# Kernel tuning notes

Hardware: AMD Instinct MI355X
Metric: run time of the kernel (lower is better)

## Reference

```python
import jax, jax.numpy as jnp
import numpy as np

B, DIM, HEADS, AGENT = 16, 256, 8, 49
POOL = 7  # int(sqrt(agent_num))


def _pool_matrix(size, out):
    # PyTorch AdaptiveAvgPool2d bin boundaries: start=floor(i*size/out), end=ceil((i+1)*size/out)
    P = np.zeros((out, size), np.float32)
    for i in range(out):
        s = (i * size) // out
        e = -((-(i + 1) * size) // out)
        P[i, s:e] = 1.0 / (e - s)
    return jnp.asarray(P)


def _forward(x, Wq, Wkv, Wproj, bproj, Wdwc, bdwc,
             an_bias, na_bias, ah_bias, aw_bias, ha_bias, wa_bias, H, W):
    b, c, h, w = x.shape
    n = H * W
    head_dim = c // HEADS
    scale = head_dim ** -0.5
    xt = x.reshape(b, c, n).transpose(0, 2, 1)            # [b, n, c]
    q = xt @ Wq.T                                          # [b, n, c]
    kv = xt @ Wkv.T
    k, v = jnp.split(kv, 2, axis=-1)
    # agent tokens: adaptive avg pool of q over the HxW grid -> 7x7
    qimg = q.reshape(b, H, W, c)
    Ph, Pw = _pool_matrix(H, POOL), _pool_matrix(W, POOL)
    agent = jnp.einsum('ph,qw,bhwc->bpqc', Ph, Pw, qimg).reshape(b, AGENT, c)

    def to_heads(t):
        return t.reshape(b, -1, HEADS, head_dim).transpose(0, 2, 1, 3)

    qh, kh, vh, ah = to_heads(q), to_heads(k), to_heads(v), to_heads(agent)

    # stage 1: agent -> kv attention with interpolated position bias
    pb1 = jax.image.resize(an_bias, (HEADS, AGENT, H, W), method='bilinear').reshape(HEADS, AGENT, n)
    pb2 = (ah_bias + aw_bias).reshape(1, HEADS, AGENT, n)
    pos_bias = pb1[None] + pb2                             # [1/b, h, 49, n]
    agent_attn = jax.nn.softmax(jnp.einsum('bhad,bhnd->bhan', ah * scale, kh) + pos_bias, axis=-1)
    agent_v = jnp.einsum('bhan,bhnd->bhad', agent_attn, vh)  # [b, h, 49, d]

    # stage 2: query -> agent attention
    ab1 = jax.image.resize(na_bias, (HEADS, AGENT, H, W), method='bilinear').reshape(HEADS, AGENT, n).transpose(0, 2, 1)
    ab2 = (ha_bias + wa_bias).reshape(1, HEADS, n, AGENT)
    agent_bias = ab1[None] + ab2                           # [1/b, h, n, 49]
    q_attn = jax.nn.softmax(jnp.einsum('bhnd,bhad->bhna', qh * scale, ah) + agent_bias, axis=-1)
    out = jnp.einsum('bhna,bhad->bhnd', q_attn, agent_v).transpose(0, 2, 1, 3).reshape(b, n, c)

    # depthwise conv residual on v
    vimg = vh.transpose(0, 2, 1, 3).reshape(b, H, W, c).transpose(0, 3, 1, 2)  # [b, c, H, W]
    dw = jax.lax.conv_general_dilated(vimg, Wdwc, (1, 1), 'SAME',
                                      feature_group_count=c,
                                      dimension_numbers=('NCHW', 'OIHW', 'NCHW'))
    dw = dw + bdwc[None, :, None, None]
    out = out + dw.transpose(0, 2, 3, 1).reshape(b, n, c)
    out = out @ Wproj.T + bproj
    return out.transpose(0, 2, 1).reshape(b, c, h, w)


def setup_inputs() -> dict:
    key = jax.random.key(0)
    ks = jax.random.split(key, 12)
    s = 0.02
    return {
        'x': jax.random.normal(ks[0], (B, DIM, 64, 64), jnp.float32),
        'Wq': jax.random.normal(ks[1], (DIM, DIM), jnp.float32) * s,
        'Wkv': jax.random.normal(ks[2], (2 * DIM, DIM), jnp.float32) * s,
        'Wproj': jax.random.normal(ks[3], (DIM, DIM), jnp.float32) * s,
        'bproj': jnp.zeros((DIM,), jnp.float32),
        'Wdwc': jax.random.normal(ks[4], (DIM, 1, 3, 3), jnp.float32) * s,
        'bdwc': jnp.zeros((DIM,), jnp.float32),
        'an_bias': jax.random.normal(ks[5], (HEADS, AGENT, 7, 7), jnp.float32) * s,
        'na_bias': jax.random.normal(ks[6], (HEADS, AGENT, 7, 7), jnp.float32) * s,
        'ah_bias': jax.random.normal(ks[7], (1, HEADS, AGENT, 64, 1), jnp.float32) * s,
        'aw_bias': jax.random.normal(ks[8], (1, HEADS, AGENT, 1, 64), jnp.float32) * s,
        'ha_bias': jax.random.normal(ks[9], (1, HEADS, 64, 1, AGENT), jnp.float32) * s,
        'wa_bias': jax.random.normal(ks[10], (1, HEADS, 1, 64, AGENT), jnp.float32) * s,
        'H': 64,
        'W': 64,
    }


def reference(x, Wq, Wkv, Wproj, bproj, Wdwc, bdwc,
              an_bias, na_bias, ah_bias, aw_bias, ha_bias, wa_bias, H, W):
    return _forward(x, Wq, Wkv, Wproj, bproj, Wdwc, bdwc,
                    an_bias, na_bias, ah_bias, aw_bias, ha_bias, wa_bias, H, W)
```

## Files before the change

kernel.cpp:

```cpp
#include <hip/hip_runtime.h>
#include <hip/hip_bf16.h>
#include <stdint.h>

using bf16 = __hip_bfloat16;

#define SCALE 0.17677669529663687f

typedef short short8 __attribute__((ext_vector_type(8)));
typedef float f32x4 __attribute__((ext_vector_type(4)));

__device__ __forceinline__ float bf2f(bf16 v) { return __bfloat162float(v); }

__device__ __forceinline__ unsigned short f2bf(float f) {
    unsigned int u = __float_as_uint(f);
    unsigned int r = u + 0x7fffu + ((u >> 16) & 1u);
    return (unsigned short)(r >> 16);
}

__device__ __forceinline__ void load8bf(const bf16* p, float* f) {
    uint4 u = *reinterpret_cast<const uint4*>(p);
    f[0] = __uint_as_float(u.x << 16); f[1] = __uint_as_float(u.x & 0xffff0000u);
    f[2] = __uint_as_float(u.y << 16); f[3] = __uint_as_float(u.y & 0xffff0000u);
    f[4] = __uint_as_float(u.z << 16); f[5] = __uint_as_float(u.z & 0xffff0000u);
    f[6] = __uint_as_float(u.w << 16); f[7] = __uint_as_float(u.w & 0xffff0000u);
}

__device__ __forceinline__ void gload16(const void* g, void* l) {
    __builtin_amdgcn_global_load_lds(
        (const __attribute__((address_space(1))) void*)g,
        (__attribute__((address_space(3))) void*)l, 16, 0, 0);
}

__global__ __launch_bounds__(256) void convert_w(
    const float* __restrict__ Wq, const float* __restrict__ Wkv,
    const float* __restrict__ Wp,
    bf16* __restrict__ Wqkv_bf, bf16* __restrict__ Wp_bf)
{
    int row = blockIdx.x, tid = threadIdx.x;
    const float* src; bf16* dst;
    if (row < 768) {
        src = (row < 256) ? Wq + (size_t)row * 256 : Wkv + (size_t)(row - 256) * 256;
        dst = Wqkv_bf + (size_t)row * 256;
    } else {
        src = Wp + (size_t)(row - 768) * 256;
        dst = Wp_bf + (size_t)(row - 768) * 256;
    }
    *reinterpret_cast<unsigned short*>(dst + tid) = f2bf(src[tid]);
}

__global__ __launch_bounds__(256) void x_to_bf16T(
    const float* __restrict__ x, bf16* __restrict__ xT)
{
    __shared__ float t[64][65];
    const int b = blockIdx.z, pos0 = blockIdx.x * 64, c0 = blockIdx.y * 64;
    const int tid = threadIdx.x;
    const int cc = tid >> 6, p = tid & 63;
    #pragma unroll
    for (int i = 0; i < 16; ++i)
        t[cc + 4 * i][p] = x[((size_t)(b * 256 + c0 + cc + 4 * i)) * 4096 + pos0 + p];
    __syncthreads();
    const int pl = tid >> 2, qd = tid & 3;
    unsigned short tmp[16];
    #pragma unroll
    for (int j = 0; j < 16; ++j) tmp[j] = f2bf(t[qd * 16 + j][pl]);
    uint4* dst = reinterpret_cast<uint4*>(xT + ((size_t)(b * 4096 + pos0 + pl)) * 256 + c0 + qd * 16);
    dst[0] = reinterpret_cast<const uint4*>(tmp)[0];
    dst[1] = reinterpret_cast<const uint4*>(tmp)[1];
}

__global__ __launch_bounds__(256) void qkv_mfma(
    const bf16* __restrict__ xT, const bf16* __restrict__ Wqkv,
    bf16* __restrict__ q, bf16* __restrict__ k, bf16* __restrict__ v)
{
    __shared__ __align__(16) short As[128 * 32];
    __shared__ __align__(16) short Bs[128 * 32];
    const int b = blockIdx.x >> 5;
    const int m0 = (blockIdx.x & 31) * 128;
    const int j0 = blockIdx.y * 128;
    const int tid = threadIdx.x;
    const int w = tid >> 6, lane = tid & 63;
    const int wm = w & 1, wn = w >> 1;
    const int quad = lane >> 4, ln = lane & 15;

    const short* Ag = (const short*)xT + ((size_t)(b * 4096 + m0)) * 256;
    const short* Bg = (const short*)Wqkv + (size_t)j0 * 256;
    const int ldrow = lane >> 2;
    const int ldcol = (lane & 3) * 8;

    f32x4 acc[4][4] = {};

    for (int k0 = 0; k0 < 256; k0 += 32) {
        __syncthreads();
        #pragma unroll
        for (int p = 0; p < 2; ++p) {
            int row = w * 32 + p * 16;
            gload16(Ag + (size_t)(row + ldrow) * 256 + k0 + ldcol, As + row * 32);
            gload16(Bg + (size_t)(row + ldrow) * 256 + k0 + ldcol, Bs + row * 32);
        }
        __syncthreads();
        short8 af[4], bfr[4];
        #pragma unroll
        for (int mi = 0; mi < 4; ++mi)
            af[mi] = *reinterpret_cast<const short8*>(&As[(wm * 64 + mi * 16 + ln) * 32 + quad * 8]);
        #pragma unroll
        for (int ni = 0; ni < 4; ++ni)
            bfr[ni] = *reinterpret_cast<const short8*>(&Bs[(wn * 64 + ni * 16 + ln) * 32 + quad * 8]);
        #pragma unroll
        for (int mi = 0; mi < 4; ++mi)
            #pragma unroll
            for (int ni = 0; ni < 4; ++ni)
                acc[mi][ni] = __builtin_amdgcn_mfma_f32_16x16x32_bf16(
                    af[mi], bfr[ni], acc[mi][ni], 0, 0, 0);
    }

    bf16* dst; int cb;
    if (j0 < 256)      { dst = q; cb = j0; }
    else if (j0 < 512) { dst = k; cb = j0 - 256; }
    else               { dst = v; cb = j0 - 512; }
    #pragma unroll
    for (int mi = 0; mi < 4; ++mi)
        #pragma unroll
        for (int r = 0; r < 4; ++r) {
            int pos = m0 + wm * 64 + mi * 16 + quad * 4 + r;
            unsigned short* o = reinterpret_cast<unsigned short*>(
                dst + ((size_t)(b * 4096 + pos)) * 256 + cb + wn * 64 + ln);
            #pragma unroll
            for (int ni = 0; ni < 4; ++ni)
                o[ni * 16] = f2bf(acc[mi][ni][r]);
        }
}

__global__ __launch_bounds__(256) void pool_agent(
    const bf16* __restrict__ q, float* __restrict__ agent)
{
    int bid = blockIdx.x;
    int b = bid / 49, a = bid % 49;
    int py = a / 7, px = a % 7;
    int ys = (py * 64) / 7, ye = ((py + 1) * 64 + 6) / 7;
    int xs = (px * 64) / 7, xe = ((px + 1) * 64 + 6) / 7;
    int ch = threadIdx.x;
    float s = 0.f;
    for (int y = ys; y < ye; ++y)
        for (int x = xs; x < xe; ++x)
            s += bf2f(q[((size_t)(b * 4096) + y * 64 + x) * 256 + ch]);
    agent[((size_t)(b * 49) + a) * 256 + ch] = s / (float)((ye - ys) * (xe - xs));
}

__global__ __launch_bounds__(256) void make_pbias(
    const float* __restrict__ an, const float* __restrict__ ahb,
    const float* __restrict__ awb, float* __restrict__ pbias)
{
    int bid = blockIdx.x;
    __shared__ float bb[49], ay[64], ax[64];
    int tid = threadIdx.x;
    if (tid < 49) bb[tid] = an[(size_t)bid * 49 + tid];
    if (tid < 64) {
        ay[tid] = ahb[(size_t)bid * 64 + tid];
        ax[tid] = awb[(size_t)bid * 64 + tid];
    }
    __syncthreads();
    for (int it = 0; it < 16; ++it) {
        int pos = it * 256 + tid;
        int y = pos >> 6, x = pos & 63;
        float fy = (y + 0.5f) * (7.f / 64.f) - 0.5f; fy = fminf(fmaxf(fy, 0.f), 6.f);
        float fx = (x + 0.5f) * (7.f / 64.f) - 0.5f; fx = fminf(fmaxf(fx, 0.f), 6.f);
        int y0 = (int)fy, x0 = (int)fx;
        int y1 = min(y0 + 1, 6), x1 = min(x0 + 1, 6);
        float wy = fy - y0, wx = fx - x0;
        float val = (1.f - wy) * ((1.f - wx) * bb[y0 * 7 + x0] + wx * bb[y0 * 7 + x1])
                  + wy * ((1.f - wx) * bb[y1 * 7 + x0] + wx * bb[y1 * 7 + x1]);
        pbias[(size_t)bid * 4096 + pos] = val + ay[y] + ax[x];
    }
}

__global__ __launch_bounds__(256) void make_abias2(
    const float* __restrict__ na, const float* __restrict__ hab,
    const float* __restrict__ wab, bf16* __restrict__ ab2)
{
    const int h = blockIdx.x, p0 = blockIdx.y * 256;
    const int tid = threadIdx.x;
    __shared__ float bb[49 * 49];
    __shared__ float hy[64 * 49];
    __shared__ float wxs[64 * 49];
    for (int i = tid; i < 49 * 49; i += 256) bb[i] = na[(size_t)h * 2401 + i];
    for (int i = tid; i < 64 * 49; i += 256) {
        hy[i]  = hab[(size_t)h * 3136 + i];
        wxs[i] = wab[(size_t)h * 3136 + i];
    }
    __syncthreads();
    const int pos = p0 + tid;
    const int y = pos >> 6, x = pos & 63;
    float fy = (y + 0.5f) * (7.f / 64.f) - 0.5f; fy = fminf(fmaxf(fy, 0.f), 6.f);
    float fx = (x + 0.5f) * (7.f / 64.f) - 0.5f; fx = fminf(fmaxf(fx, 0.f), 6.f);
    int y0 = (int)fy, x0 = (int)fx;
    int y1 = min(y0 + 1, 6), x1 = min(x0 + 1, 6);
    float wy = fy - y0, wxv = fx - x0;
    float w00 = (1.f - wy) * (1.f - wxv), w01 = (1.f - wy) * wxv;
    float w10 = wy * (1.f - wxv),        w11 = wy * wxv;
    int g00 = y0 * 7 + x0, g01 = y0 * 7 + x1, g10 = y1 * 7 + x0, g11 = y1 * 7 + x1;
    unsigned short outv[64];
    #pragma unroll
    for (int a = 0; a < 49; ++a) {
        float val = w00 * bb[a * 49 + g00] + w01 * bb[a * 49 + g01]
                  + w10 * bb[a * 49 + g10] + w11 * bb[a * 49 + g11]
                  + hy[y * 49 + a] + wxs[x * 49 + a];
        outv[a] = f2bf(val);
    }
    #pragma unroll
    for (int a = 49; a < 64; ++a) outv[a] = 0;
    uint4* dst = reinterpret_cast<uint4*>(
        reinterpret_cast<unsigned short*>(ab2) + ((size_t)(h * 4096) + pos) * 64);
    #pragma unroll
    for (int j = 0; j < 8; ++j) dst[j] = reinterpret_cast<const uint4*>(outv)[j];
}

__global__ __launch_bounds__(256) void stage1(
    const float* __restrict__ agent, const bf16* __restrict__ k,
    const bf16* __restrict__ v, const float* __restrict__ pbias,
    float* __restrict__ part_O, float* __restrict__ part_sum)
{
    const int bid = blockIdx.x;
    const int split = bid & 7, h = (bid >> 3) & 7, b = bid >> 6;
    const int tid = threadIdx.x;
    const int w = tid >> 6, lane = tid & 63;
    const int ln = lane & 15, quad = lane >> 4;

    __shared__ __align__(16) short agLds[64 * 32];
    __shared__ __align__(16) short pLds[64 * 140];
    __shared__ __align__(16) short vtLds[32 * 140];

    for (int i = tid; i < 64 * 32; i += 256) {
        int a = i >> 5, d = i & 31;
        float val = (a < 49) ? agent[((size_t)(b * 49) + a) * 256 + h * 32 + d] : 0.f;
        agLds[i] = (short)f2bf(val);
    }
    __syncthreads();

    const short8 agFrag = *reinterpret_cast<const short8*>(&agLds[(w * 16 + ln) * 32 + quad * 8]);
    const int a_row = w * 16 + quad * 4;

    f32x4 oAcc[2] = {};
    float sacc[4] = {0.f, 0.f, 0.f, 0.f};
    const f32x4 zero4 = {0.f, 0.f, 0.f, 0.f};

    for (int sub = 0; sub < 4; ++sub) {
        const int nbase = split * 512 + sub * 128;
        __syncthreads();
        {
            const int n_loc = tid & 127, dh = (tid >> 7) * 16;
            const short* vr = (const short*)v + ((size_t)(b * 4096) + nbase + n_loc) * 256 + h * 32 + dh;
            uint4 u0 = *reinterpret_cast<const uint4*>(vr);
            uint4 u1 = *reinterpret_cast<const uint4*>(vr + 8);
            unsigned int uu[8] = {u0.x, u0.y, u0.z, u0.w, u1.x, u1.y, u1.z, u1.w};
            #pragma unroll
            for (int j = 0; j < 8; ++j) {
                vtLds[(dh + 2 * j) * 140 + n_loc]     = (short)(uu[j] & 0xffffu);
                vtLds[(dh + 2 * j + 1) * 140 + n_loc] = (short)(uu[j] >> 16);
            }
        }
        short8 kf[8];
        #pragma unroll
        for (int t = 0; t < 8; ++t) {
            int n = nbase + t * 16 + ln;
            kf[t] = *reinterpret_cast<const short8*>(
                (const short*)k + ((size_t)(b * 4096) + n) * 256 + h * 32 + quad * 8);
        }
        #pragma unroll
        for (int t = 0; t < 8; ++t) {
            f32x4 s = __builtin_amdgcn_mfma_f32_16x16x32_bf16(agFrag, kf[t], zero4, 0, 0, 0);
            int n = nbase + t * 16 + ln;
            #pragma unroll
            for (int r = 0; r < 4; ++r) {
                int a = a_row + r;
                float e = 0.f;
                if (a < 49) {
                    float sv = s[r] * SCALE + pbias[((size_t)(h * 49) + a) * 4096 + n];
                    e = __expf(sv);
                }
                sacc[r] += e;
                pLds[(a_row + r) * 140 + t * 16 + ln] = (short)f2bf(e);
            }
        }
        __syncthreads();
        #pragma unroll
        for (int ks = 0; ks < 4; ++ks) {
            short8 pf = *reinterpret_cast<const short8*>(&pLds[(w * 16 + ln) * 140 + ks * 32 + quad * 8]);
            #pragma unroll
            for (int dt = 0; dt < 2; ++dt) {
                short8 vf = *reinterpret_cast<const short8*>(&vtLds[(dt * 16 + ln) * 140 + ks * 32 + quad * 8]);
                oAcc[dt] = __builtin_amdgcn_mfma_f32_16x16x32_bf16(pf, vf, oAcc[dt], 0, 0, 0);
            }
        }
    }

    const size_t obase = ((size_t)((b * 8 + h) * 8 + split)) * 1568;
    #pragma unroll
    for (int dt = 0; dt < 2; ++dt)
        #pragma unroll
        for (int r = 0; r < 4; ++r) {
            int a = a_row + r;
            if (a < 49)
                part_O[obase + a * 32 + dt * 16 + ln] = oAcc[dt][r];
        }
    #pragma unroll
    for (int r = 0; r < 4; ++r) {
        float sv = sacc[r];
        #pragma unroll
        for (int m = 1; m < 16; m <<= 1) sv += __shfl_xor(sv, m, 64);
        if (ln == 0) {
            int a = a_row + r;
            if (a < 49)
                part_sum[((b * 8 + h) * 8 + split) * 49 + a] = sv;
        }
    }
}

__global__ __launch_bounds__(256) void stage1_fin(
    const float* __restrict__ part_O, const float* __restrict__ part_sum,
    bf16* __restrict__ avT)
{
    int bh = blockIdx.x;
    __shared__ float inv[49];
    int tid = threadIdx.x;
    if (tid < 49) {
        float s = 0.f;
        #pragma unroll
        for (int sp = 0; sp < 8; ++sp) s += part_sum[(bh * 8 + sp) * 49 + tid];
        inv[tid] = 1.f / s;
    }
    __syncthreads();
    unsigned short* dst = reinterpret_cast<unsigned short*>(avT) + (size_t)bh * 2048;
    for (int i = tid; i < 2048; i += 256) {
        int d = i >> 6, a = i & 63;
        float val = 0.f;
        if (a < 49) {
            float o = 0.f;
            #pragma unroll
            for (int sp = 0; sp < 8; ++sp)
                o += part_O[((size_t)(bh * 8) + sp) * 1568 + a * 32 + d];
            val = o * inv[a];
        }
        dst[i] = f2bf(val);
    }
}

__global__ __launch_bounds__(256) void stage2_mfma(
    const bf16* __restrict__ q, const bf16* __restrict__ v,
    const float* __restrict__ agent, const bf16* __restrict__ avT,
    const bf16* __restrict__ ab2, const float* __restrict__ wdwc,
    const float* __restrict__ bdwc, bf16* __restrict__ mid)
{
    const int bh = blockIdx.x;
    const int b = bh >> 3, h = bh & 7;
    const int base = blockIdx.y * 256;
    const int tid = threadIdx.x;
    const int w = tid >> 6, lane = tid & 63;
    const int quad = lane >> 4, ln = lane & 15;

    __shared__ __align__(16) short agLds[64 * 32];
    __shared__ __align__(16) short pLds[4][16 * 72];
    __shared__ __align__(16) float oLds[64 * 36];
    __shared__ float wdLds[32 * 9];
    __shared__ float bdLds[32];

    for (int i = tid; i < 64 * 32; i += 256) {
        int a = i >> 5, d = i & 31;
        float val = (a < 49) ? agent[((size_t)(b * 49) + a) * 256 + h * 32 + d] : 0.f;
        agLds[i] = (short)f2bf(val);
    }
    for (int i = tid; i < 288; i += 256) wdLds[i] = wdwc[(size_t)(h * 32) * 9 + i];
    if (tid < 32) bdLds[tid] = bdwc[h * 32 + tid];
    __syncthreads();

    short8 agF[4];
    #pragma unroll
    for (int t = 0; t < 4; ++t)
        agF[t] = *reinterpret_cast<const short8*>(&agLds[(t * 16 + ln) * 32 + quad * 8]);

    short8 avF[2][2];
    #pragma unroll
    for (int dt = 0; dt < 2; ++dt)
        #pragma unroll
        for (int kc = 0; kc < 2; ++kc)
            avF[dt][kc] = *reinterpret_cast<const short8*>(
                (const short*)avT + ((size_t)bh * 32 + dt * 16 + ln) * 64 + kc * 32 + quad * 8);

    const int prow = tid >> 2, cl = (tid & 3) * 8;
    const f32x4 zero4 = {0.f, 0.f, 0.f, 0.f};

    for (int sub = 0; sub < 4; ++sub) {
        const int pos0w = base + sub * 64 + w * 16;
        short8 qf = *reinterpret_cast<const short8*>(
            (const short*)q + ((size_t)(b * 4096) + pos0w + ln) * 256 + h * 32 + quad * 8);
        f32x4 sT[4];
        #pragma unroll
        for (int t = 0; t < 4; ++t)
            sT[t] = __builtin_amdgcn_mfma_f32_16x16x32_bf16(qf, agF[t], zero4, 0, 0, 0);
        float e[4][4];
        float part[4] = {0.f, 0.f, 0.f, 0.f};
        #pragma unroll
        for (int t = 0; t < 4; ++t) {
            int a = t * 16 + ln;
            #pragma unroll
            for (int r = 0; r < 4; ++r) {
                float ev = 0.f;
                if (a < 49) {
                    int pos = pos0w + quad * 4 + r;
                    float bias = bf2f(ab2[((size_t)(h * 4096) + pos) * 64 + a]);
                    ev = __expf(sT[t][r] * SCALE + bias);
                }
                e[t][r] = ev;
                part[r] += ev;
            }
        }
        #pragma unroll
        for (int r = 0; r < 4; ++r) {
            #pragma unroll
            for (int m = 1; m < 16; m <<= 1) part[r] += __shfl_xor(part[r], m, 64);
            part[r] = 1.f / part[r];
        }
        #pragma unroll
        for (int t = 0; t < 4; ++t)
            #pragma unroll
            for (int r = 0; r < 4; ++r)
                pLds[w][(quad * 4 + r) * 72 + t * 16 + ln] = (short)f2bf(e[t][r] * part[r]);
        __syncthreads();
        f32x4 oAcc[2] = {};
        #pragma unroll
        for (int kc = 0; kc < 2; ++kc) {
            short8 pf = *reinterpret_cast<const short8*>(&pLds[w][ln * 72 + kc * 32 + quad * 8]);
            #pragma unroll
            for (int dt = 0; dt < 2; ++dt)
                oAcc[dt] = __builtin_amdgcn_mfma_f32_16x16x32_bf16(pf, avF[dt][kc], oAcc[dt], 0, 0, 0);
        }
        #pragma unroll
        for (int dt = 0; dt < 2; ++dt)
            #pragma unroll
            for (int r = 0; r < 4; ++r)
                oLds[(w * 16 + quad * 4 + r) * 36 + dt * 16 + ln] = oAcc[dt][r];
        __syncthreads();
        {
            int pos = base + sub * 64 + prow;
            float acc[8];
            #pragma unroll
            for (int j = 0; j < 8; ++j) acc[j] = oLds[prow * 36 + cl + j] + bdLds[cl + j];
            int y = pos >> 6, x = pos & 63;
            #pragma unroll
            for (int dy = -1; dy <= 1; ++dy) {
                int yy = y + dy; if (yy < 0 || yy > 63) continue;
                #pragma unroll
                for (int dx = -1; dx <= 1; ++dx) {
                    int xx = x + dx; if (xx < 0 || xx > 63) continue;
                    int widx = (dy + 1) * 3 + (dx + 1);
                    const bf16* vr = v + ((size_t)(b * 4096) + yy * 64 + xx) * 256 + h * 32 + cl;
                    float f[8]; load8bf(vr, f);
                    #pragma unroll
                    for (int j = 0; j < 8; ++j)
                        acc[j] = fmaf(wdLds[(cl + j) * 9 + widx], f[j], acc[j]);
                }
            }
            unsigned short o16[8];
            #pragma unroll
            for (int j = 0; j < 8; ++j) o16[j] = f2bf(acc[j]);
            *reinterpret_cast<uint4*>(mid + ((size_t)(b * 4096) + pos) * 256 + h * 32 + cl) =
                *reinterpret_cast<const uint4*>(o16);
        }
    }
}

__global__ __launch_bounds__(256) void proj_mfma(
    const bf16* __restrict__ mid, const bf16* __restrict__ Wp,
    const float* __restrict__ bp, float* __restrict__ out)
{
    __shared__ __align__(16) short As[128 * 32];
    __shared__ __align__(16) short Bs[128 * 32];
    const int m0 = blockIdx.x * 128;
    const int b  = blockIdx.y >> 5;
    const int n0 = (blockIdx.y & 31) * 128;
    const int tid = threadIdx.x;
    const int w = tid >> 6, lane = tid & 63;
    const int wm = w & 1, wn = w >> 1;
    const int quad = lane >> 4, ln = lane & 15;

    const short* Ag = (const short*)Wp + (size_t)m0 * 256;
    const short* Bg = (const short*)mid + ((size_t)(b * 4096 + n0)) * 256;
    const int ldrow = lane >> 2;
    const int ldcol = (lane & 3) * 8;

    f32x4 acc[4][4] = {};

    for (int k0 = 0; k0 < 256; k0 += 32) {
        __syncthreads();
        #pragma unroll
        for (int p = 0; p < 2; ++p) {
            int row = w * 32 + p * 16;
            gload16(Ag + (size_t)(row + ldrow) * 256 + k0 + ldcol, As + row * 32);
            gload16(Bg + (size_t)(row + ldrow) * 256 + k0 + ldcol, Bs + row * 32);
        }
        __syncthreads();
        short8 af[4], bfr[4];
        #pragma unroll
        for (int mi = 0; mi < 4; ++mi)
            af[mi] = *reinterpret_cast<const short8*>(&As[(wm * 64 + mi * 16 + ln) * 32 + quad * 8]);
        #pragma unroll
        for (int ni = 0; ni < 4; ++ni)
            bfr[ni] = *reinterpret_cast<const short8*>(&Bs[(wn * 64 + ni * 16 + ln) * 32 + quad * 8]);
        #pragma unroll
        for (int mi = 0; mi < 4; ++mi)
            #pragma unroll
            for (int ni = 0; ni < 4; ++ni)
                acc[mi][ni] = __builtin_amdgcn_mfma_f32_16x16x32_bf16(
                    af[mi], bfr[ni], acc[mi][ni], 0, 0, 0);
    }

    #pragma unroll
    for (int mi = 0; mi < 4; ++mi)
        #pragma unroll
        for (int r = 0; r < 4; ++r) {
            int ch = m0 + wm * 64 + mi * 16 + quad * 4 + r;
            float bias = bp[ch];
            float* o = out + ((size_t)(b * 256 + ch)) * 4096 + n0 + wn * 64 + ln;
            #pragma unroll
            for (int ni = 0; ni < 4; ++ni)
                o[ni * 16] = acc[mi][ni][r] + bias;
        }
}

extern "C" void kernel_launch(void* const* d_in, const int* in_sizes, int n_in,
                              void* d_out, int out_size, void* d_ws, size_t ws_size,
                              hipStream_t stream)
{
    const float* x       = (const float*)d_in[0];
    const float* Wq      = (const float*)d_in[1];
    const float* Wkv     = (const float*)d_in[2];
    const float* Wproj   = (const float*)d_in[3];
    const float* bproj   = (const float*)d_in[4];
    const float* Wdwc    = (const float*)d_in[5];
    const float* bdwc    = (const float*)d_in[6];
    const float* an_bias = (const float*)d_in[7];
    const float* na_bias = (const float*)d_in[8];
    const float* ah_bias = (const float*)d_in[9];
    const float* aw_bias = (const float*)d_in[10];
    const float* ha_bias = (const float*)d_in[11];
    const float* wa_bias = (const float*)d_in[12];

    char* ws = (char*)d_ws;
    bf16*  q      = (bf16*)(ws + 0);
    bf16*  k      = (bf16*)(ws + 33554432);
    bf16*  v      = (bf16*)(ws + 67108864);
    bf16*  xT     = (bf16*)(ws + 100663296);
    float* part_O   = (float*)(ws + 100663296);
    float* part_sum = (float*)(ws + 100663296 + 6422528);
    bf16*  mid    = (bf16*)(ws + 100663296);
    float* agent  = (float*)(ws + 134217728);
    bf16*  avT    = (bf16*)(ws + 135020544);
    float* pbias  = (float*)(ws + 135823360);
    bf16*  ab2    = (bf16*)(ws + 142245888);
    bf16*  Wqkv_bf = (bf16*)(ws + 148668416);
    bf16*  Wp_bf   = (bf16*)(ws + 149061632);
    float* out    = (float*)d_out;

    convert_w  <<<dim3(1024),      256, 0, stream>>>(Wq, Wkv, Wproj, Wqkv_bf, Wp_bf);
    x_to_bf16T <<<dim3(64, 4, 16), 256, 0, stream>>>(x, xT);
    qkv_mfma   <<<dim3(512, 6),    256, 0, stream>>>(xT, Wqkv_bf, q, k, v);
    pool_agent <<<dim3(784),       256, 0, stream>>>(q, agent);
    make_pbias <<<dim3(392),       256, 0, stream>>>(an_bias, ah_bias, aw_bias, pbias);
    make_abias2<<<dim3(8, 16),     256, 0, stream>>>(na_bias, ha_bias, wa_bias, ab2);
    stage1     <<<dim3(1024),      256, 0, stream>>>(agent, k, v, pbias, part_O, part_sum);
    stage1_fin <<<dim3(128),       256, 0, stream>>>(part_O, part_sum, avT);
    stage2_mfma<<<dim3(128, 16),   256, 0, stream>>>(q, v, agent, avT, ab2, Wdwc, bdwc, mid);
    proj_mfma  <<<dim3(2, 512),    256, 0, stream>>>(mid, Wp_bf, bproj, out);
}
```

Measured before the change: 387.3 us.

## Prefetch conv taps and bias, permute bias layout, double-buffer output LDS in stage2

```diff
diff --git a/kernel.cpp b/kernel.cpp
--- a/kernel.cpp
+++ b/kernel.cpp
@@ -200,14 +200,14 @@
     int g00 = y0 * 7 + x0, g01 = y0 * 7 + x1, g10 = y1 * 7 + x0, g11 = y1 * 7 + x1;
     unsigned short outv[64];
     #pragma unroll
-    for (int a = 0; a < 49; ++a) {
-        float val = w00 * bb[a * 49 + g00] + w01 * bb[a * 49 + g01]
-                  + w10 * bb[a * 49 + g10] + w11 * bb[a * 49 + g11]
-                  + hy[y * 49 + a] + wxs[x * 49 + a];
-        outv[a] = f2bf(val);
-    }
-    #pragma unroll
-    for (int a = 49; a < 64; ++a) outv[a] = 0;
+    for (int a = 0; a < 64; ++a) {
+        float val = 0.f;
+        if (a < 49)
+            val = w00 * bb[a * 49 + g00] + w01 * bb[a * 49 + g01]
+                + w10 * bb[a * 49 + g10] + w11 * bb[a * 49 + g11]
+                + hy[y * 49 + a] + wxs[x * 49 + a];
+        outv[(a & 15) * 4 + (a >> 4)] = f2bf(val);
+    }
     uint4* dst = reinterpret_cast<uint4*>(
         reinterpret_cast<unsigned short*>(ab2) + ((size_t)(h * 4096) + pos) * 64);
     #pragma unroll
@@ -359,7 +359,7 @@
 
     __shared__ __align__(16) short agLds[64 * 32];
     __shared__ __align__(16) short pLds[4][16 * 72];
-    __shared__ __align__(16) float oLds[64 * 36];
+    __shared__ __align__(16) float oLds[2][64 * 36];
     __shared__ float wdLds[32 * 9];
     __shared__ float bdLds[32];
 
@@ -389,26 +389,54 @@
     const f32x4 zero4 = {0.f, 0.f, 0.f, 0.f};
 
     for (int sub = 0; sub < 4; ++sub) {
+        const int p = sub & 1;
         const int pos0w = base + sub * 64 + w * 16;
+
+        const int posd = base + sub * 64 + prow;
+        const int yd = posd >> 6, xd = posd & 63;
+        uint4 vpre[9];
+        #pragma unroll
+        for (int dy = -1; dy <= 1; ++dy)
+            #pragma unroll
+            for (int dx = -1; dx <= 1; ++dx) {
+                int idx = (dy + 1) * 3 + (dx + 1);
+                int yy = yd + dy, xx = xd + dx;
+                int yc = min(max(yy, 0), 63), xc = min(max(xx, 0), 63);
+                uint4 t = *reinterpret_cast<const uint4*>(
+                    v + ((size_t)(b * 4096) + yc * 64 + xc) * 256 + h * 32 + cl);
+                if ((unsigned)yy >= 64u || (unsigned)xx >= 64u) { t.x = 0; t.y = 0; t.z = 0; t.w = 0; }
+                vpre[idx] = t;
+            }
+
+        uint2 bpre[4];
+        #pragma unroll
+        for (int r = 0; r < 4; ++r) {
+            int posr = pos0w + quad * 4 + r;
+            bpre[r] = *reinterpret_cast<const uint2*>(
+                reinterpret_cast<const unsigned short*>(ab2) + ((size_t)(h * 4096) + posr) * 64 + ln * 4);
+        }
+
         short8 qf = *reinterpret_cast<const short8*>(
             (const short*)q + ((size_t)(b * 4096) + pos0w + ln) * 256 + h * 32 + quad * 8);
         f32x4 sT[4];
         #pragma unroll
         for (int t = 0; t < 4; ++t)
             sT[t] = __builtin_amdgcn_mfma_f32_16x16x32_bf16(qf, agF[t], zero4, 0, 0, 0);
+
         float e[4][4];
         float part[4] = {0.f, 0.f, 0.f, 0.f};
         #pragma unroll
-        for (int t = 0; t < 4; ++t) {
-            int a = t * 16 + ln;
-            #pragma unroll
-            for (int r = 0; r < 4; ++r) {
+        for (int r = 0; r < 4; ++r) {
+            float bias[4];
+            bias[0] = __uint_as_float(bpre[r].x << 16);
+            bias[1] = __uint_as_float(bpre[r].x & 0xffff0000u);
+            bias[2] = __uint_as_float(bpre[r].y << 16);
+            bias[3] = __uint_as_float(bpre[r].y & 0xffff0000u);
+            #pragma unroll
+            for (int t = 0; t < 4; ++t) {
+                int a = t * 16 + ln;
                 float ev = 0.f;
-                if (a < 49) {
-                    int pos = pos0w + quad * 4 + r;
-                    float bias = bf2f(ab2[((size_t)(h * 4096) + pos) * 64 + a]);
-                    ev = __expf(sT[t][r] * SCALE + bias);
-                }
+                if (a < 49) ev = __expf(sT[t][r] * SCALE + bias[t]);
                 e[t][r] = ev;
                 part[r] += ev;
             }
@@ -419,12 +447,13 @@
             for (int m = 1; m < 16; m <<= 1) part[r] += __shfl_xor(part[r], m, 64);
             part[r] = 1.f / part[r];
         }
+
         #pragma unroll
         for (int t = 0; t < 4; ++t)
             #pragma unroll
             for (int r = 0; r < 4; ++r)
                 pLds[w][(quad * 4 + r) * 72 + t * 16 + ln] = (short)f2bf(e[t][r] * part[r]);
-        __syncthreads();
+
         f32x4 oAcc[2] = {};
         #pragma unroll
         for (int kc = 0; kc < 2; ++kc) {
@@ -433,36 +462,34 @@
             for (int dt = 0; dt < 2; ++dt)
                 oAcc[dt] = __builtin_amdgcn_mfma_f32_16x16x32_bf16(pf, avF[dt][kc], oAcc[dt], 0, 0, 0);
         }
+
         #pragma unroll
         for (int dt = 0; dt < 2; ++dt)
             #pragma unroll
             for (int r = 0; r < 4; ++r)
-                oLds[(w * 16 + quad * 4 + r) * 36 + dt * 16 + ln] = oAcc[dt][r];
+                oLds[p][(w * 16 + quad * 4 + r) * 36 + dt * 16 + ln] = oAcc[dt][r];
         __syncthreads();
+
         {
-            int pos = base + sub * 64 + prow;
             float acc[8];
             #pragma unroll
-            for (int j = 0; j < 8; ++j) acc[j] = oLds[prow * 36 + cl + j] + bdLds[cl + j];
-            int y = pos >> 6, x = pos & 63;
-            #pragma unroll
-            for (int dy = -1; dy <= 1; ++dy) {
-                int yy = y + dy; if (yy < 0 || yy > 63) continue;
+            for (int j = 0; j < 8; ++j) acc[j] = oLds[p][prow * 36 + cl + j] + bdLds[cl + j];
+            #pragma unroll
+            for (int idx = 0; idx < 9; ++idx) {
+                unsigned int uu[4] = {vpre[idx].x, vpre[idx].y, vpre[idx].z, vpre[idx].w};
+                float f[8];
+                f[0] = __uint_as_float(uu[0] << 16); f[1] = __uint_as_float(uu[0] & 0xffff0000u);
+                f[2] = __uint_as_float(uu[1] << 16); f[3] = __uint_as_float(uu[1] & 0xffff0000u);
+                f[4] = __uint_as_float(uu[2] << 16); f[5] = __uint_as_float(uu[2] & 0xffff0000u);
+                f[6] = __uint_as_float(uu[3] << 16); f[7] = __uint_as_float(uu[3] & 0xffff0000u);
                 #pragma unroll
-                for (int dx = -1; dx <= 1; ++dx) {
-                    int xx = x + dx; if (xx < 0 || xx > 63) continue;
-                    int widx = (dy + 1) * 3 + (dx + 1);
-                    const bf16* vr = v + ((size_t)(b * 4096) + yy * 64 + xx) * 256 + h * 32 + cl;
-                    float f[8]; load8bf(vr, f);
-                    #pragma unroll
-                    for (int j = 0; j < 8; ++j)
-                        acc[j] = fmaf(wdLds[(cl + j) * 9 + widx], f[j], acc[j]);
-                }
+                for (int j = 0; j < 8; ++j)
+                    acc[j] = fmaf(wdLds[(cl + j) * 9 + idx], f[j], acc[j]);
             }
             unsigned short o16[8];
             #pragma unroll
             for (int j = 0; j < 8; ++j) o16[j] = f2bf(acc[j]);
-            *reinterpret_cast<uint4*>(mid + ((size_t)(b * 4096) + pos) * 256 + h * 32 + cl) =
+            *reinterpret_cast<uint4*>(mid + ((size_t)(b * 4096) + posd) * 256 + h * 32 + cl) =
                 *reinterpret_cast<const uint4*>(o16);
         }
     }
```

Result: faster. 371.8 us (-4.0%).
